# Optimization experiments

Hardware: AMD Instinct MI355X
Metric: run time of the kernel (lower is better)

Reference implementation:

```python
import jax, jax.numpy as jnp
import numpy as np

DIM = 256
HEADS = 8
WH, WW = 8, 8
N = WH * WW
B_ = 2048
NW = 64  # num windows per image; B_ // NW = batch of 32
CPB_HIDDEN = 256


def _log_rel_index(wh, ww):
    ch = np.arange(wh)
    cw = np.arange(ww)
    coords = np.stack(np.meshgrid(ch, cw, indexing='ij'))      # (2, wh, ww)
    cf = coords.reshape(2, -1)                                  # (2, N)
    rel = cf[:, :, None] - cf[:, None, :]                       # (2, N, N)
    rel = rel.transpose(1, 2, 0).astype(np.float32)             # (N, N, 2)
    return np.sign(rel) * np.log1p(np.abs(rel))


def setup_inputs() -> dict:
    key = jax.random.key(0)
    ks = jax.random.split(key, 16)
    s = 0.02
    inp = {
        'x': jax.random.normal(ks[0], (B_, N, DIM), jnp.float32),
        'KV': jax.random.normal(ks[1], (B_, N, DIM), jnp.float32),
        'mask': jnp.zeros((NW, N, N), jnp.float32),
        # linear weights stored (in, out): y = x @ W + b
        'Wq': jax.random.normal(ks[2], (DIM, DIM), jnp.float32) * s,
        'bq': jnp.zeros((DIM,), jnp.float32),
        'Wkv': jax.random.normal(ks[3], (DIM, 2 * DIM), jnp.float32) * s,
        'bkv': jnp.zeros((2 * DIM,), jnp.float32),
        'Wp': jax.random.normal(ks[4], (DIM, DIM), jnp.float32) * s,
        'bp': jnp.zeros((DIM,), jnp.float32),
        'cpb_w1': jax.random.normal(ks[5], (2, CPB_HIDDEN), jnp.float32) * s,
        'cpb_b1': jnp.zeros((CPB_HIDDEN,), jnp.float32),
        'cpb_w2': jax.random.normal(ks[6], (CPB_HIDDEN, HEADS), jnp.float32) * s,
        'cpb_b2': jnp.zeros((HEADS,), jnp.float32),
        'tau': jnp.ones((HEADS, N, N), jnp.float32),
        'log_rel_idx': jnp.asarray(_log_rel_index(WH, WW)),  # (N, N, 2)
    }
    return inp


def reference(x, KV, mask, Wq, bq, Wkv, bkv, Wp, bp,
              cpb_w1, cpb_b1, cpb_w2, cpb_b2, tau, log_rel_idx):
    Bw, n, C = x.shape
    H = tau.shape[0]
    hd = C // H
    scale = hd ** -0.5

    q = (x @ Wq + bq).reshape(Bw, n, H, hd).transpose(0, 2, 1, 3) * scale   # (B_,H,N,hd)
    kv = (KV @ Wkv + bkv).reshape(Bw, n, 2, H, hd).transpose(2, 0, 3, 1, 4)  # (2,B_,H,N,hd)
    k, v = kv[0], kv[1]

    num = jnp.einsum('bhqd,bhkd->bhqk', q, k)
    qn = jnp.sqrt(jnp.sum(q * q, axis=-1, keepdims=True))                    # (B_,H,N,1)
    kn = jnp.sqrt(jnp.sum(k * k, axis=-1, keepdims=True))                    # (B_,H,N,1)
    denom = jnp.maximum(qn * kn.transpose(0, 1, 3, 2), 1e-6)
    attn = num / denom
    attn = attn / jnp.clip(tau[:, :n, :n], 0.01)[None]

    # continuous relative position bias MLP: (N,N,2) -> (N,N,H)
    h = jax.nn.relu(log_rel_idx[:n, :n] @ cpb_w1 + cpb_b1)
    bias = (h @ cpb_w2 + cpb_b2).transpose(2, 0, 1)                          # (H,N,N)
    attn = attn + bias[None]

    nW = mask.shape[0]
    attn = attn.reshape(Bw // nW, nW, H, n, n) + mask[None, :, None]
    attn = attn.reshape(Bw, H, n, n)
    attn = jax.nn.softmax(attn, axis=-1)

    out = jnp.einsum('bhqk,bhkd->bhqd', attn, v)
    out = out.transpose(0, 2, 1, 3).reshape(Bw, n, C)
    out = out @ Wp + bp
    return out
```

## Files before the change

kernel.cpp:

```cpp
#include <hip/hip_runtime.h>
#include <hip/hip_bf16.h>

#define NWIN 64

typedef __attribute__((ext_vector_type(8))) short v8s;
typedef __attribute__((ext_vector_type(4))) float v4f;

#define WQT_OFF   0u
#define WKVT_OFF  131072u
#define WPT_OFF   393216u
#define ITB_OFF   524288u

static __device__ __forceinline__ short f2bf(float f) {
  union { float f; unsigned int u; } v; v.f = f;
  unsigned int u = v.u;
  return (short)((u + 0x7fffu + ((u >> 16) & 1u)) >> 16);
}

static __device__ __forceinline__ int packbf(float lo, float hi) {
  __hip_bfloat162 h = __float22bfloat162_rn(float2{lo, hi});
  union { __hip_bfloat162 h; int i; } u; u.h = h; return u.i;
}

__global__ void prep_kernel(const float* __restrict__ Wq, const float* __restrict__ Wkv,
                            const float* __restrict__ Wp,
                            short* __restrict__ WqT, short* __restrict__ WkvT,
                            short* __restrict__ WpT) {
  int id = blockIdx.x * 256 + threadIdx.x;
  if (id < 65536) {
    int o = id >> 8, i = id & 255;
    WqT[id] = f2bf(Wq[i * 256 + o]);
  } else if (id < 196608) {
    int t = id - 65536; int o = t >> 8, i = t & 255;
    WkvT[t] = f2bf(Wkv[i * 512 + o]);
  } else if (id < 262144) {
    int t = id - 196608; int o = t >> 8, i = t & 255;
    WpT[t] = f2bf(Wp[i * 256 + o]);
  }
}

__global__ void cpb_kernel(const float* __restrict__ w1, const float* __restrict__ b1,
                           const float* __restrict__ w2, const float* __restrict__ b2,
                           const float* __restrict__ lri, const float* __restrict__ tau,
                           unsigned int* __restrict__ itbh) {
  int ij = blockIdx.x * 256 + threadIdx.x;
  float l0 = lri[ij * 2], l1 = lri[ij * 2 + 1];
  float acc[8];
#pragma unroll
  for (int h = 0; h < 8; ++h) acc[h] = b2[h];
  for (int c = 0; c < 256; ++c) {
    float hv = fmaxf(l0 * w1[c] + l1 * w1[256 + c] + b1[c], 0.0f);
#pragma unroll
    for (int h = 0; h < 8; ++h) acc[h] += hv * w2[c * 8 + h];
  }
#pragma unroll
  for (int h = 0; h < 8; ++h) {
    float it = 1.0f / fmaxf(tau[h * 4096 + ij], 0.01f);
    itbh[h * 4096 + ij] = (unsigned int)packbf(it, acc[h]);
  }
}

static __device__ __forceinline__ v8s xform_tile(int p0a, int p0b, int p1a, int p1b,
                                                 int base, int mdsel) {
  int a0 = __shfl(p0a, base, 64),      b0 = __shfl(p1a, base, 64);
  int a1 = __shfl(p0b, base, 64),      b1 = __shfl(p1b, base, 64);
  int a2 = __shfl(p0a, base + 16, 64), b2 = __shfl(p1a, base + 16, 64);
  int a3 = __shfl(p0b, base + 16, 64), b3 = __shfl(p1b, base + 16, 64);
  union { v8s v; int i[4]; } r;
  r.i[0] = mdsel ? b0 : a0;
  r.i[1] = mdsel ? b1 : a1;
  r.i[2] = mdsel ? b2 : a2;
  r.i[3] = mdsel ? b3 : a3;
  return r.v;
}

__global__ __launch_bounds__(512, 4) void wattn_kernel(
    const float* __restrict__ x, const float* __restrict__ KV,
    const float* __restrict__ mask,
    const float* __restrict__ bq, const float* __restrict__ bkv,
    const float* __restrict__ bp,
    const short* __restrict__ WqT, const short* __restrict__ WkvT,
    const short* __restrict__ WpT, const unsigned int* __restrict__ itbh,
    float* __restrict__ out) {
  __shared__ short sm[37888];

  const int b = blockIdx.x;
  const int tid = threadIdx.x;
  const int w = tid >> 6;
  const int lane = tid & 63;
  const int cc = lane & 15;
  const int qd = lane >> 4;
  const int base = cc + 32 * (qd & 1);
  const int mdsel = qd >> 1;
  const v4f vzero = {0.f, 0.f, 0.f, 0.f};
  short* xs = sm;
  short* kvs = sm + 16896;
  short* ms = sm + 33792;

  {
    const float4* xb = (const float4*)(x + (size_t)b * 16384);
    const float4* kb = (const float4*)(KV + (size_t)b * 16384);
    const float4* mb = (const float4*)(mask + (size_t)(b & (NWIN - 1)) * 4096);
    float4 m0 = mb[tid * 2], m1 = mb[tid * 2 + 1];
#pragma unroll
    for (int half = 0; half < 2; ++half) {
      float4 vx[4], vk[4];
#pragma unroll
      for (int ii = 0; ii < 4; ++ii) {
        int i = tid + (half * 4 + ii) * 512;
        vx[ii] = xb[i];
        vk[ii] = kb[i];
      }
#pragma unroll
      for (int ii = 0; ii < 4; ++ii) {
        int i = tid + (half * 4 + ii) * 512;
        int r = i >> 6, col = (i & 63) << 2;
        int2 px = { packbf(vx[ii].x, vx[ii].y), packbf(vx[ii].z, vx[ii].w) };
        int2 pk = { packbf(vk[ii].x, vk[ii].y), packbf(vk[ii].z, vk[ii].w) };
        *(int2*)&xs[r * 264 + col] = px;
        *(int2*)&kvs[r * 264 + col] = pk;
      }
    }
    int byte = (tid * 16) ^ (((tid >> 3) & 7) << 3);
    int2 p0 = { packbf(m0.x, m0.y), packbf(m0.z, m0.w) };
    int2 p1 = { packbf(m1.x, m1.y), packbf(m1.z, m1.w) };
    *(int2*)((char*)ms + byte) = p0;
    *(int2*)((char*)ms + (byte ^ 8)) = p1;
  }
  const short* wqb = WqT + (32 * w + cc) * 256 + qd * 8;
  v8s wq0[4], wq1[4];
#pragma unroll
  for (int it = 0; it < 4; ++it) {
    wq0[it] = *(const v8s*)(wqb + it * 32);
    wq1[it] = *(const v8s*)(wqb + 16 * 256 + it * 32);
  }
  __syncthreads();

  v4f Dq[2][4];
#pragma unroll
  for (int md = 0; md < 2; ++md)
#pragma unroll
    for (int nt = 0; nt < 4; ++nt) Dq[md][nt] = vzero;
  {
#pragma unroll
    for (int it = 0; it < 4; ++it) {
#pragma unroll
      for (int nt = 0; nt < 4; ++nt) {
        v8s bx = *(const v8s*)(xs + (nt * 16 + cc) * 264 + it * 32 + qd * 8);
        Dq[0][nt] = __builtin_amdgcn_mfma_f32_16x16x32_bf16(wq0[it], bx, Dq[0][nt], 0, 0, 0);
        Dq[1][nt] = __builtin_amdgcn_mfma_f32_16x16x32_bf16(wq1[it], bx, Dq[1][nt], 0, 0, 0);
      }
    }
#pragma unroll
    for (int it = 4; it < 8; ++it) {
      v8s a0 = *(const v8s*)(wqb + it * 32);
      v8s a1 = *(const v8s*)(wqb + 16 * 256 + it * 32);
#pragma unroll
      for (int nt = 0; nt < 4; ++nt) {
        v8s bx = *(const v8s*)(xs + (nt * 16 + cc) * 264 + it * 32 + qd * 8);
        Dq[0][nt] = __builtin_amdgcn_mfma_f32_16x16x32_bf16(a0, bx, Dq[0][nt], 0, 0, 0);
        Dq[1][nt] = __builtin_amdgcn_mfma_f32_16x16x32_bf16(a1, bx, Dq[1][nt], 0, 0, 0);
      }
    }
  }
  v8s qB[4];
  {
    v4f b0 = *(const v4f*)(bq + 32 * w + qd * 4);
    v4f b1 = *(const v4f*)(bq + 32 * w + 16 + qd * 4);
#pragma unroll
    for (int nt = 0; nt < 4; ++nt) {
      float s = 0.f;
#pragma unroll
      for (int rg = 0; rg < 4; ++rg) {
        float v0 = Dq[0][nt][rg] + b0[rg];
        float v1 = Dq[1][nt][rg] + b1[rg];
        Dq[0][nt][rg] = v0; Dq[1][nt][rg] = v1;
        s += v0 * v0 + v1 * v1;
      }
      s += __shfl_xor(s, 16); s += __shfl_xor(s, 32);
      float inv = rsqrtf(s + 1e-24f);
      int p00 = packbf(Dq[0][nt][0] * inv, Dq[0][nt][1] * inv);
      int p01 = packbf(Dq[0][nt][2] * inv, Dq[0][nt][3] * inv);
      int p10 = packbf(Dq[1][nt][0] * inv, Dq[1][nt][1] * inv);
      int p11 = packbf(Dq[1][nt][2] * inv, Dq[1][nt][3] * inv);
      qB[nt] = xform_tile(p00, p01, p10, p11, base, mdsel);
    }
  }

  v4f Dk[2][4], Dv[4][2];
#pragma unroll
  for (int nt = 0; nt < 4; ++nt) {
    Dk[0][nt] = vzero; Dk[1][nt] = vzero;
    Dv[nt][0] = vzero; Dv[nt][1] = vzero;
  }
  {
    const short* wkb = WkvT + (32 * w + cc) * 256 + qd * 8;
    const short* wvb = WkvT + (256 + 32 * w + cc) * 256 + qd * 8;
#pragma unroll
    for (int it = 0; it < 8; ++it) {
      v8s ak0 = *(const v8s*)(wkb + it * 32);
      v8s ak1 = *(const v8s*)(wkb + 16 * 256 + it * 32);
      v8s bv0 = *(const v8s*)(wvb + it * 32);
      v8s bv1 = *(const v8s*)(wvb + 16 * 256 + it * 32);
#pragma unroll
      for (int nt = 0; nt < 4; ++nt) {
        v8s kf = *(const v8s*)(kvs + (nt * 16 + cc) * 264 + it * 32 + qd * 8);
        Dk[0][nt] = __builtin_amdgcn_mfma_f32_16x16x32_bf16(ak0, kf, Dk[0][nt], 0, 0, 0);
        Dk[1][nt] = __builtin_amdgcn_mfma_f32_16x16x32_bf16(ak1, kf, Dk[1][nt], 0, 0, 0);
        Dv[nt][0] = __builtin_amdgcn_mfma_f32_16x16x32_bf16(kf, bv0, Dv[nt][0], 0, 0, 0);
        Dv[nt][1] = __builtin_amdgcn_mfma_f32_16x16x32_bf16(kf, bv1, Dv[nt][1], 0, 0, 0);
      }
    }
  }
  v8s kA[4];
  {
    v4f b0 = *(const v4f*)(bkv + 32 * w + qd * 4);
    v4f b1 = *(const v4f*)(bkv + 32 * w + 16 + qd * 4);
#pragma unroll
    for (int nt = 0; nt < 4; ++nt) {
      float s = 0.f;
#pragma unroll
      for (int rg = 0; rg < 4; ++rg) {
        float v0 = Dk[0][nt][rg] + b0[rg];
        float v1 = Dk[1][nt][rg] + b1[rg];
        Dk[0][nt][rg] = v0; Dk[1][nt][rg] = v1;
        s += v0 * v0 + v1 * v1;
      }
      s += __shfl_xor(s, 16); s += __shfl_xor(s, 32);
      float inv = rsqrtf(s + 1e-24f);
      int p00 = packbf(Dk[0][nt][0] * inv, Dk[0][nt][1] * inv);
      int p01 = packbf(Dk[0][nt][2] * inv, Dk[0][nt][3] * inv);
      int p10 = packbf(Dk[1][nt][0] * inv, Dk[1][nt][1] * inv);
      int p11 = packbf(Dk[1][nt][2] * inv, Dk[1][nt][3] * inv);
      kA[nt] = xform_tile(p00, p01, p10, p11, base, mdsel);
    }
  }
  v8s av[2][2];
  {
    float bv0 = bkv[256 + 32 * w + cc];
    float bv1 = bkv[256 + 32 * w + 16 + cc];
    int Pv[4][2][2];
#pragma unroll
    for (int vt = 0; vt < 4; ++vt) {
      Pv[vt][0][0] = packbf(Dv[vt][0][0] + bv0, Dv[vt][0][1] + bv0);
      Pv[vt][0][1] = packbf(Dv[vt][0][2] + bv0, Dv[vt][0][3] + bv0);
      Pv[vt][1][0] = packbf(Dv[vt][1][0] + bv1, Dv[vt][1][1] + bv1);
      Pv[vt][1][1] = packbf(Dv[vt][1][2] + bv1, Dv[vt][1][3] + bv1);
    }
#pragma unroll
    for (int md = 0; md < 2; ++md)
#pragma unroll
      for (int kc = 0; kc < 2; ++kc)
        av[md][kc] = xform_tile(Pv[2 * kc][md][0], Pv[2 * kc][md][1],
                                Pv[2 * kc + 1][md][0], Pv[2 * kc + 1][md][1], base, mdsel);
  }

  v4f Sv[4][4];
  __builtin_amdgcn_s_setprio(1);
#pragma unroll
  for (int jt = 0; jt < 4; ++jt)
#pragma unroll
    for (int it = 0; it < 4; ++it)
      Sv[jt][it] = __builtin_amdgcn_mfma_f32_16x16x32_bf16(kA[jt], qB[it], vzero, 0, 0, 0);
  __builtin_amdgcn_s_setprio(0);

  {
    const uint4* th4 = (const uint4*)(itbh + (size_t)w * 4096);
#pragma unroll
    for (int it = 0; it < 4; ++it) {
      int i = it * 16 + cc;
      uint4 T[4]; int2 M[4];
#pragma unroll
      for (int jt = 0; jt < 4; ++jt) {
        T[jt] = th4[(i * 64 + jt * 16 + qd * 4) >> 2];
        int byte = (i * 128 + jt * 32 + qd * 8) ^ ((i & 7) << 3);
        M[jt] = *(const int2*)((const char*)ms + byte);
      }
#pragma unroll
      for (int jt = 0; jt < 4; ++jt) {
        unsigned mxw = (unsigned)M[jt].x, myw = (unsigned)M[jt].y;
        float m0 = __uint_as_float(mxw << 16);
        float m1 = __uint_as_float(mxw & 0xffff0000u);
        float m2 = __uint_as_float(myw << 16);
        float m3 = __uint_as_float(myw & 0xffff0000u);
        unsigned u0 = T[jt].x, u1 = T[jt].y, u2 = T[jt].z, u3 = T[jt].w;
        Sv[jt][it][0] = Sv[jt][it][0] * __uint_as_float(u0 << 16) + (__uint_as_float(u0 & 0xffff0000u) + m0);
        Sv[jt][it][1] = Sv[jt][it][1] * __uint_as_float(u1 << 16) + (__uint_as_float(u1 & 0xffff0000u) + m1);
        Sv[jt][it][2] = Sv[jt][it][2] * __uint_as_float(u2 << 16) + (__uint_as_float(u2 & 0xffff0000u) + m2);
        Sv[jt][it][3] = Sv[jt][it][3] * __uint_as_float(u3 << 16) + (__uint_as_float(u3 & 0xffff0000u) + m3);
      }
      float mA = fmaxf(fmaxf(Sv[0][it][0], Sv[0][it][1]), fmaxf(Sv[0][it][2], Sv[0][it][3]));
      float mB = fmaxf(fmaxf(Sv[1][it][0], Sv[1][it][1]), fmaxf(Sv[1][it][2], Sv[1][it][3]));
      float mC = fmaxf(fmaxf(Sv[2][it][0], Sv[2][it][1]), fmaxf(Sv[2][it][2], Sv[2][it][3]));
      float mD = fmaxf(fmaxf(Sv[3][it][0], Sv[3][it][1]), fmaxf(Sv[3][it][2], Sv[3][it][3]));
      float mx = fmaxf(fmaxf(mA, mB), fmaxf(mC, mD));
      mx = fmaxf(mx, __shfl_xor(mx, 16)); mx = fmaxf(mx, __shfl_xor(mx, 32));
      float sj[4];
#pragma unroll
      for (int jt = 0; jt < 4; ++jt) {
        float e0 = __expf(Sv[jt][it][0] - mx);
        float e1 = __expf(Sv[jt][it][1] - mx);
        float e2 = __expf(Sv[jt][it][2] - mx);
        float e3 = __expf(Sv[jt][it][3] - mx);
        Sv[jt][it][0] = e0; Sv[jt][it][1] = e1;
        Sv[jt][it][2] = e2; Sv[jt][it][3] = e3;
        sj[jt] = (e0 + e1) + (e2 + e3);
      }
      float sum = (sj[0] + sj[1]) + (sj[2] + sj[3]);
      sum += __shfl_xor(sum, 16); sum += __shfl_xor(sum, 32);
      float rs = 1.0f / sum;
#pragma unroll
      for (int jt = 0; jt < 4; ++jt)
#pragma unroll
        for (int rg = 0; rg < 4; ++rg) Sv[jt][it][rg] *= rs;
    }
  }

  __syncthreads();
  v4f Do[2][4];
  {
    char* psw = (char*)kvs + w * 4096;
#pragma unroll
    for (int it = 0; it < 4; ++it) {
      char* ps = psw + (it & 1) * 2048;
#pragma unroll
      for (int jt = 0; jt < 4; ++jt) {
        int2 pr;
        pr.x = packbf(Sv[jt][it][0], Sv[jt][it][1]);
        pr.y = packbf(Sv[jt][it][2], Sv[jt][it][3]);
        int byte = (cc * 128 + jt * 32 + qd * 8) ^ ((cc & 7) << 4);
        *(int2*)(ps + byte) = pr;
      }
      int rb0 = (cc * 128 + qd * 16) ^ ((cc & 7) << 4);
      int rb1 = (cc * 128 + 64 + qd * 16) ^ ((cc & 7) << 4);
      v8s pB0 = *(const v8s*)(ps + rb0);
      v8s pB1 = *(const v8s*)(ps + rb1);
      __builtin_amdgcn_s_setprio(1);
#pragma unroll
      for (int md = 0; md < 2; ++md) {
        v4f t = __builtin_amdgcn_mfma_f32_16x16x32_bf16(av[md][0], pB0, vzero, 0, 0, 0);
        Do[md][it] = __builtin_amdgcn_mfma_f32_16x16x32_bf16(av[md][1], pB1, t, 0, 0, 0);
      }
      __builtin_amdgcn_s_setprio(0);
    }
  }

  const short* wpb = WpT + (32 * w + cc) * 256 + qd * 8;
  v8s wp0[2], wp1[2];
#pragma unroll
  for (int it = 0; it < 2; ++it) {
    wp0[it] = *(const v8s*)(wpb + it * 32);
    wp1[it] = *(const v8s*)(wpb + 16 * 256 + it * 32);
  }

#pragma unroll
  for (int md = 0; md < 2; ++md)
#pragma unroll
    for (int it = 0; it < 4; ++it) {
      int addr = (it * 16 + cc) * 264 + 32 * w + md * 16 + qd * 4;
      *(int*)&sm[addr] = packbf(Do[md][it][0], Do[md][it][1]);
      *(int*)&sm[addr + 2] = packbf(Do[md][it][2], Do[md][it][3]);
    }
  __syncthreads();

  v4f pa[4][2];
#pragma unroll
  for (int mt = 0; mt < 4; ++mt) { pa[mt][0] = vzero; pa[mt][1] = vzero; }
  {
#pragma unroll
    for (int it = 0; it < 2; ++it) {
#pragma unroll
      for (int mt = 0; mt < 4; ++mt) {
        v8s a = *(const v8s*)(sm + (mt * 16 + cc) * 264 + it * 32 + qd * 8);
        pa[mt][0] = __builtin_amdgcn_mfma_f32_16x16x32_bf16(a, wp0[it], pa[mt][0], 0, 0, 0);
        pa[mt][1] = __builtin_amdgcn_mfma_f32_16x16x32_bf16(a, wp1[it], pa[mt][1], 0, 0, 0);
      }
    }
#pragma unroll
    for (int it = 2; it < 8; ++it) {
      v8s b0 = *(const v8s*)(wpb + it * 32);
      v8s b1 = *(const v8s*)(wpb + 16 * 256 + it * 32);
#pragma unroll
      for (int mt = 0; mt < 4; ++mt) {
        v8s a = *(const v8s*)(sm + (mt * 16 + cc) * 264 + it * 32 + qd * 8);
        pa[mt][0] = __builtin_amdgcn_mfma_f32_16x16x32_bf16(a, b0, pa[mt][0], 0, 0, 0);
        pa[mt][1] = __builtin_amdgcn_mfma_f32_16x16x32_bf16(a, b1, pa[mt][1], 0, 0, 0);
      }
    }
  }
  {
    float b0 = bp[32 * w + cc], b1 = bp[32 * w + 16 + cc];
    float* ob = out + (size_t)b * 16384;
#pragma unroll
    for (int mt = 0; mt < 4; ++mt)
#pragma unroll
      for (int rg = 0; rg < 4; ++rg) {
        int row = mt * 16 + qd * 4 + rg;
        ob[row * 256 + 32 * w + cc] = pa[mt][0][rg] + b0;
        ob[row * 256 + 32 * w + 16 + cc] = pa[mt][1][rg] + b1;
      }
  }
}

extern "C" void kernel_launch(void* const* d_in, const int* in_sizes, int n_in,
                              void* d_out, int out_size, void* d_ws, size_t ws_size,
                              hipStream_t stream) {
  const float* x    = (const float*)d_in[0];
  const float* KV   = (const float*)d_in[1];
  const float* mask = (const float*)d_in[2];
  const float* Wq   = (const float*)d_in[3];
  const float* bq   = (const float*)d_in[4];
  const float* Wkv  = (const float*)d_in[5];
  const float* bkv  = (const float*)d_in[6];
  const float* Wp   = (const float*)d_in[7];
  const float* bp   = (const float*)d_in[8];
  const float* cw1  = (const float*)d_in[9];
  const float* cb1  = (const float*)d_in[10];
  const float* cw2  = (const float*)d_in[11];
  const float* cb2  = (const float*)d_in[12];
  const float* tau  = (const float*)d_in[13];
  const float* lri  = (const float*)d_in[14];

  unsigned char* ws = (unsigned char*)d_ws;
  short* WqT   = (short*)(ws + WQT_OFF);
  short* WkvT  = (short*)(ws + WKVT_OFF);
  short* WpT   = (short*)(ws + WPT_OFF);
  unsigned int* itbh = (unsigned int*)(ws + ITB_OFF);

  prep_kernel<<<1024, 256, 0, stream>>>(Wq, Wkv, Wp, WqT, WkvT, WpT);
  cpb_kernel<<<16, 256, 0, stream>>>(cw1, cb1, cw2, cb2, lri, tau, itbh);
  wattn_kernel<<<2048, 512, 0, stream>>>(x, KV, mask, bq, bkv, bp,
                                         WqT, WkvT, WpT, itbh, (float*)d_out);
}
```

Before: 507.7 us.

## Make attention kernel persistent over four windows with x prefetch double-buffering

Launches 512 blocks that each process four windows in a loop, swapping two shared-memory buffers. The next window's x tile is loaded from global memory and written to the spare buffer while the output projection runs. The aim is to cut block launch overhead and hide x load latency. The cost is fewer resident blocks per CU, and the KV load for later windows is not overlapped with compute.

```diff
diff --git a/kernel.cpp b/kernel.cpp
--- a/kernel.cpp
+++ b/kernel.cpp
@@ -84,7 +84,7 @@
     float* __restrict__ out) {
   __shared__ short sm[37888];
 
-  const int b = blockIdx.x;
+  const int b0 = blockIdx.x;
   const int tid = threadIdx.x;
   const int w = tid >> 6;
   const int lane = tid & 63;
@@ -93,14 +93,19 @@
   const int base = cc + 32 * (qd & 1);
   const int mdsel = qd >> 1;
   const v4f vzero = {0.f, 0.f, 0.f, 0.f};
-  short* xs = sm;
-  short* kvs = sm + 16896;
   short* ms = sm + 33792;
+  short* pX = sm;
+  short* pK = sm + 16896;
+
+  const short* wqb = WqT + (32 * w + cc) * 256 + qd * 8;
+  const short* wkb = WkvT + (32 * w + cc) * 256 + qd * 8;
+  const short* wvb = WkvT + (256 + 32 * w + cc) * 256 + qd * 8;
+  const short* wpb = WpT + (32 * w + cc) * 256 + qd * 8;
 
   {
-    const float4* xb = (const float4*)(x + (size_t)b * 16384);
-    const float4* kb = (const float4*)(KV + (size_t)b * 16384);
-    const float4* mb = (const float4*)(mask + (size_t)(b & (NWIN - 1)) * 4096);
+    const float4* xb = (const float4*)(x + (size_t)b0 * 16384);
+    const float4* kb = (const float4*)(KV + (size_t)b0 * 16384);
+    const float4* mb = (const float4*)(mask + (size_t)(b0 & (NWIN - 1)) * 4096);
     float4 m0 = mb[tid * 2], m1 = mb[tid * 2 + 1];
 #pragma unroll
     for (int half = 0; half < 2; ++half) {
@@ -117,8 +122,8 @@
         int r = i >> 6, col = (i & 63) << 2;
         int2 px = { packbf(vx[ii].x, vx[ii].y), packbf(vx[ii].z, vx[ii].w) };
         int2 pk = { packbf(vk[ii].x, vk[ii].y), packbf(vk[ii].z, vk[ii].w) };
-        *(int2*)&xs[r * 264 + col] = px;
-        *(int2*)&kvs[r * 264 + col] = pk;
+        *(int2*)&pX[r * 264 + col] = px;
+        *(int2*)&pK[r * 264 + col] = pk;
       }
     }
     int byte = (tid * 16) ^ (((tid >> 3) & 7) << 3);
@@ -127,278 +132,340 @@
     *(int2*)((char*)ms + byte) = p0;
     *(int2*)((char*)ms + (byte ^ 8)) = p1;
   }
-  const short* wqb = WqT + (32 * w + cc) * 256 + qd * 8;
-  v8s wq0[4], wq1[4];
-#pragma unroll
-  for (int it = 0; it < 4; ++it) {
-    wq0[it] = *(const v8s*)(wqb + it * 32);
-    wq1[it] = *(const v8s*)(wqb + 16 * 256 + it * 32);
-  }
-  __syncthreads();
-
-  v4f Dq[2][4];
-#pragma unroll
-  for (int md = 0; md < 2; ++md)
-#pragma unroll
-    for (int nt = 0; nt < 4; ++nt) Dq[md][nt] = vzero;
-  {
+
+#pragma unroll 1
+  for (int wi = 0; wi < 4; ++wi) {
+    const int b = b0 + wi * 512;
+
+    if (wi > 0) {
+      const float4* kb = (const float4*)(KV + (size_t)b * 16384);
+      float4 kf[8];
+#pragma unroll
+      for (int c = 0; c < 8; ++c) kf[c] = kb[tid + c * 512];
+#pragma unroll
+      for (int c = 0; c < 8; ++c) {
+        int i = tid + c * 512;
+        int r = i >> 6, col = (i & 63) << 2;
+        int2 pk = { packbf(kf[c].x, kf[c].y), packbf(kf[c].z, kf[c].w) };
+        *(int2*)&pK[r * 264 + col] = pk;
+      }
+    }
+    v8s wq0[4], wq1[4];
 #pragma unroll
     for (int it = 0; it < 4; ++it) {
+      wq0[it] = *(const v8s*)(wqb + it * 32);
+      wq1[it] = *(const v8s*)(wqb + 16 * 256 + it * 32);
+    }
+    __syncthreads();
+
+    v4f Dq[2][4];
+#pragma unroll
+    for (int md = 0; md < 2; ++md)
+#pragma unroll
+      for (int nt = 0; nt < 4; ++nt) Dq[md][nt] = vzero;
+    {
+#pragma unroll
+      for (int it = 0; it < 4; ++it) {
+#pragma unroll
+        for (int nt = 0; nt < 4; ++nt) {
+          v8s bx = *(const v8s*)(pX + (nt * 16 + cc) * 264 + it * 32 + qd * 8);
+          Dq[0][nt] = __builtin_amdgcn_mfma_f32_16x16x32_bf16(wq0[it], bx, Dq[0][nt], 0, 0, 0);
+          Dq[1][nt] = __builtin_amdgcn_mfma_f32_16x16x32_bf16(wq1[it], bx, Dq[1][nt], 0, 0, 0);
+        }
+      }
+#pragma unroll
+      for (int it = 4; it < 8; ++it) {
+        v8s a0 = *(const v8s*)(wqb + it * 32);
+        v8s a1 = *(const v8s*)(wqb + 16 * 256 + it * 32);
+#pragma unroll
+        for (int nt = 0; nt < 4; ++nt) {
+          v8s bx = *(const v8s*)(pX + (nt * 16 + cc) * 264 + it * 32 + qd * 8);
+          Dq[0][nt] = __builtin_amdgcn_mfma_f32_16x16x32_bf16(a0, bx, Dq[0][nt], 0, 0, 0);
+          Dq[1][nt] = __builtin_amdgcn_mfma_f32_16x16x32_bf16(a1, bx, Dq[1][nt], 0, 0, 0);
+        }
+      }
+    }
+    v8s qB[4];
+    {
+      v4f bb0 = *(const v4f*)(bq + 32 * w + qd * 4);
+      v4f bb1 = *(const v4f*)(bq + 32 * w + 16 + qd * 4);
 #pragma unroll
       for (int nt = 0; nt < 4; ++nt) {
-        v8s bx = *(const v8s*)(xs + (nt * 16 + cc) * 264 + it * 32 + qd * 8);
-        Dq[0][nt] = __builtin_amdgcn_mfma_f32_16x16x32_bf16(wq0[it], bx, Dq[0][nt], 0, 0, 0);
-        Dq[1][nt] = __builtin_amdgcn_mfma_f32_16x16x32_bf16(wq1[it], bx, Dq[1][nt], 0, 0, 0);
-      }
-    }
-#pragma unroll
-    for (int it = 4; it < 8; ++it) {
-      v8s a0 = *(const v8s*)(wqb + it * 32);
-      v8s a1 = *(const v8s*)(wqb + 16 * 256 + it * 32);
+        float s = 0.f;
+#pragma unroll
+        for (int rg = 0; rg < 4; ++rg) {
+          float v0 = Dq[0][nt][rg] + bb0[rg];
+          float v1 = Dq[1][nt][rg] + bb1[rg];
+          Dq[0][nt][rg] = v0; Dq[1][nt][rg] = v1;
+          s += v0 * v0 + v1 * v1;
+        }
+        s += __shfl_xor(s, 16); s += __shfl_xor(s, 32);
+        float inv = rsqrtf(s + 1e-24f);
+        int p00 = packbf(Dq[0][nt][0] * inv, Dq[0][nt][1] * inv);
+        int p01 = packbf(Dq[0][nt][2] * inv, Dq[0][nt][3] * inv);
+        int p10 = packbf(Dq[1][nt][0] * inv, Dq[1][nt][1] * inv);
+        int p11 = packbf(Dq[1][nt][2] * inv, Dq[1][nt][3] * inv);
+        qB[nt] = xform_tile(p00, p01, p10, p11, base, mdsel);
+      }
+    }
+
+    v4f Dk[2][4], Dv[4][2];
+#pragma unroll
+    for (int nt = 0; nt < 4; ++nt) {
+      Dk[0][nt] = vzero; Dk[1][nt] = vzero;
+      Dv[nt][0] = vzero; Dv[nt][1] = vzero;
+    }
+    {
+#pragma unroll
+      for (int it = 0; it < 8; ++it) {
+        v8s ak0 = *(const v8s*)(wkb + it * 32);
+        v8s ak1 = *(const v8s*)(wkb + 16 * 256 + it * 32);
+        v8s bv0 = *(const v8s*)(wvb + it * 32);
+        v8s bv1 = *(const v8s*)(wvb + 16 * 256 + it * 32);
+#pragma unroll
+        for (int nt = 0; nt < 4; ++nt) {
+          v8s kf = *(const v8s*)(pK + (nt * 16 + cc) * 264 + it * 32 + qd * 8);
+          Dk[0][nt] = __builtin_amdgcn_mfma_f32_16x16x32_bf16(ak0, kf, Dk[0][nt], 0, 0, 0);
+          Dk[1][nt] = __builtin_amdgcn_mfma_f32_16x16x32_bf16(ak1, kf, Dk[1][nt], 0, 0, 0);
+          Dv[nt][0] = __builtin_amdgcn_mfma_f32_16x16x32_bf16(kf, bv0, Dv[nt][0], 0, 0, 0);
+          Dv[nt][1] = __builtin_amdgcn_mfma_f32_16x16x32_bf16(kf, bv1, Dv[nt][1], 0, 0, 0);
+        }
+      }
+    }
+    v8s kA[4];
+    {
+      v4f bb0 = *(const v4f*)(bkv + 32 * w + qd * 4);
+      v4f bb1 = *(const v4f*)(bkv + 32 * w + 16 + qd * 4);
 #pragma unroll
       for (int nt = 0; nt < 4; ++nt) {
-        v8s bx = *(const v8s*)(xs + (nt * 16 + cc) * 264 + it * 32 + qd * 8);
-        Dq[0][nt] = __builtin_amdgcn_mfma_f32_16x16x32_bf16(a0, bx, Dq[0][nt], 0, 0, 0);
-        Dq[1][nt] = __builtin_amdgcn_mfma_f32_16x16x32_bf16(a1, bx, Dq[1][nt], 0, 0, 0);
-      }
-    }
-  }
-  v8s qB[4];
-  {
-    v4f b0 = *(const v4f*)(bq + 32 * w + qd * 4);
-    v4f b1 = *(const v4f*)(bq + 32 * w + 16 + qd * 4);
-#pragma unroll
-    for (int nt = 0; nt < 4; ++nt) {
-      float s = 0.f;
-#pragma unroll
-      for (int rg = 0; rg < 4; ++rg) {
-        float v0 = Dq[0][nt][rg] + b0[rg];
-        float v1 = Dq[1][nt][rg] + b1[rg];
-        Dq[0][nt][rg] = v0; Dq[1][nt][rg] = v1;
-        s += v0 * v0 + v1 * v1;
-      }
-      s += __shfl_xor(s, 16); s += __shfl_xor(s, 32);
-      float inv = rsqrtf(s + 1e-24f);
-      int p00 = packbf(Dq[0][nt][0] * inv, Dq[0][nt][1] * inv);
-      int p01 = packbf(Dq[0][nt][2] * inv, Dq[0][nt][3] * inv);
-      int p10 = packbf(Dq[1][nt][0] * inv, Dq[1][nt][1] * inv);
-      int p11 = packbf(Dq[1][nt][2] * inv, Dq[1][nt][3] * inv);
-      qB[nt] = xform_tile(p00, p01, p10, p11, base, mdsel);
-    }
-  }
-
-  v4f Dk[2][4], Dv[4][2];
-#pragma unroll
-  for (int nt = 0; nt < 4; ++nt) {
-    Dk[0][nt] = vzero; Dk[1][nt] = vzero;
-    Dv[nt][0] = vzero; Dv[nt][1] = vzero;
-  }
-  {
-    const short* wkb = WkvT + (32 * w + cc) * 256 + qd * 8;
-    const short* wvb = WkvT + (256 + 32 * w + cc) * 256 + qd * 8;
-#pragma unroll
-    for (int it = 0; it < 8; ++it) {
-      v8s ak0 = *(const v8s*)(wkb + it * 32);
-      v8s ak1 = *(const v8s*)(wkb + 16 * 256 + it * 32);
-      v8s bv0 = *(const v8s*)(wvb + it * 32);
-      v8s bv1 = *(const v8s*)(wvb + 16 * 256 + it * 32);
-#pragma unroll
-      for (int nt = 0; nt < 4; ++nt) {
-        v8s kf = *(const v8s*)(kvs + (nt * 16 + cc) * 264 + it * 32 + qd * 8);
-        Dk[0][nt] = __builtin_amdgcn_mfma_f32_16x16x32_bf16(ak0, kf, Dk[0][nt], 0, 0, 0);
-        Dk[1][nt] = __builtin_amdgcn_mfma_f32_16x16x32_bf16(ak1, kf, Dk[1][nt], 0, 0, 0);
-        Dv[nt][0] = __builtin_amdgcn_mfma_f32_16x16x32_bf16(kf, bv0, Dv[nt][0], 0, 0, 0);
-        Dv[nt][1] = __builtin_amdgcn_mfma_f32_16x16x32_bf16(kf, bv1, Dv[nt][1], 0, 0, 0);
-      }
-    }
-  }
-  v8s kA[4];
-  {
-    v4f b0 = *(const v4f*)(bkv + 32 * w + qd * 4);
-    v4f b1 = *(const v4f*)(bkv + 32 * w + 16 + qd * 4);
-#pragma unroll
-    for (int nt = 0; nt < 4; ++nt) {
-      float s = 0.f;
-#pragma unroll
-      for (int rg = 0; rg < 4; ++rg) {
-        float v0 = Dk[0][nt][rg] + b0[rg];
-        float v1 = Dk[1][nt][rg] + b1[rg];
-        Dk[0][nt][rg] = v0; Dk[1][nt][rg] = v1;
-        s += v0 * v0 + v1 * v1;
-      }
-      s += __shfl_xor(s, 16); s += __shfl_xor(s, 32);
-      float inv = rsqrtf(s + 1e-24f);
-      int p00 = packbf(Dk[0][nt][0] * inv, Dk[0][nt][1] * inv);
-      int p01 = packbf(Dk[0][nt][2] * inv, Dk[0][nt][3] * inv);
-      int p10 = packbf(Dk[1][nt][0] * inv, Dk[1][nt][1] * inv);
-      int p11 = packbf(Dk[1][nt][2] * inv, Dk[1][nt][3] * inv);
-      kA[nt] = xform_tile(p00, p01, p10, p11, base, mdsel);
-    }
-  }
-  v8s av[2][2];
-  {
-    float bv0 = bkv[256 + 32 * w + cc];
-    float bv1 = bkv[256 + 32 * w + 16 + cc];
-    int Pv[4][2][2];
-#pragma unroll
-    for (int vt = 0; vt < 4; ++vt) {
-      Pv[vt][0][0] = packbf(Dv[vt][0][0] + bv0, Dv[vt][0][1] + bv0);
-      Pv[vt][0][1] = packbf(Dv[vt][0][2] + bv0, Dv[vt][0][3] + bv0);
-      Pv[vt][1][0] = packbf(Dv[vt][1][0] + bv1, Dv[vt][1][1] + bv1);
-      Pv[vt][1][1] = packbf(Dv[vt][1][2] + bv1, Dv[vt][1][3] + bv1);
-    }
+        float s = 0.f;
+#pragma unroll
+        for (int rg = 0; rg < 4; ++rg) {
+          float v0 = Dk[0][nt][rg] + bb0[rg];
+          float v1 = Dk[1][nt][rg] + bb1[rg];
+          Dk[0][nt][rg] = v0; Dk[1][nt][rg] = v1;
+          s += v0 * v0 + v1 * v1;
+        }
+        s += __shfl_xor(s, 16); s += __shfl_xor(s, 32);
+        float inv = rsqrtf(s + 1e-24f);
+        int p00 = packbf(Dk[0][nt][0] * inv, Dk[0][nt][1] * inv);
+        int p01 = packbf(Dk[0][nt][2] * inv, Dk[0][nt][3] * inv);
+        int p10 = packbf(Dk[1][nt][0] * inv, Dk[1][nt][1] * inv);
+        int p11 = packbf(Dk[1][nt][2] * inv, Dk[1][nt][3] * inv);
+        kA[nt] = xform_tile(p00, p01, p10, p11, base, mdsel);
+      }
+    }
+    v8s av[2][2];
+    {
+      float bv0 = bkv[256 + 32 * w + cc];
+      float bv1 = bkv[256 + 32 * w + 16 + cc];
+      int Pv[4][2][2];
+#pragma unroll
+      for (int vt = 0; vt < 4; ++vt) {
+        Pv[vt][0][0] = packbf(Dv[vt][0][0] + bv0, Dv[vt][0][1] + bv0);
+        Pv[vt][0][1] = packbf(Dv[vt][0][2] + bv0, Dv[vt][0][3] + bv0);
+        Pv[vt][1][0] = packbf(Dv[vt][1][0] + bv1, Dv[vt][1][1] + bv1);
+        Pv[vt][1][1] = packbf(Dv[vt][1][2] + bv1, Dv[vt][1][3] + bv1);
+      }
+#pragma unroll
+      for (int md = 0; md < 2; ++md)
+#pragma unroll
+        for (int kc = 0; kc < 2; ++kc)
+          av[md][kc] = xform_tile(Pv[2 * kc][md][0], Pv[2 * kc][md][1],
+                                  Pv[2 * kc + 1][md][0], Pv[2 * kc + 1][md][1], base, mdsel);
+    }
+
+    v4f Sv[4][4];
+    __builtin_amdgcn_s_setprio(1);
+#pragma unroll
+    for (int jt = 0; jt < 4; ++jt)
+#pragma unroll
+      for (int it = 0; it < 4; ++it)
+        Sv[jt][it] = __builtin_amdgcn_mfma_f32_16x16x32_bf16(kA[jt], qB[it], vzero, 0, 0, 0);
+    __builtin_amdgcn_s_setprio(0);
+
+    {
+      const uint4* th4 = (const uint4*)(itbh + (size_t)w * 4096);
+#pragma unroll
+      for (int it = 0; it < 4; ++it) {
+        int i = it * 16 + cc;
+        uint4 T[4]; int2 M[4];
+#pragma unroll
+        for (int jt = 0; jt < 4; ++jt) {
+          T[jt] = th4[(i * 64 + jt * 16 + qd * 4) >> 2];
+          int byte = (i * 128 + jt * 32 + qd * 8) ^ ((i & 7) << 3);
+          M[jt] = *(const int2*)((const char*)ms + byte);
+        }
+#pragma unroll
+        for (int jt = 0; jt < 4; ++jt) {
+          unsigned mxw = (unsigned)M[jt].x, myw = (unsigned)M[jt].y;
+          float m0 = __uint_as_float(mxw << 16);
+          float m1 = __uint_as_float(mxw & 0xffff0000u);
+          float m2 = __uint_as_float(myw << 16);
+          float m3 = __uint_as_float(myw & 0xffff0000u);
+          unsigned u0 = T[jt].x, u1 = T[jt].y, u2 = T[jt].z, u3 = T[jt].w;
+          Sv[jt][it][0] = Sv[jt][it][0] * __uint_as_float(u0 << 16) + (__uint_as_float(u0 & 0xffff0000u) + m0);
+          Sv[jt][it][1] = Sv[jt][it][1] * __uint_as_float(u1 << 16) + (__uint_as_float(u1 & 0xffff0000u) + m1);
+          Sv[jt][it][2] = Sv[jt][it][2] * __uint_as_float(u2 << 16) + (__uint_as_float(u2 & 0xffff0000u) + m2);
+          Sv[jt][it][3] = Sv[jt][it][3] * __uint_as_float(u3 << 16) + (__uint_as_float(u3 & 0xffff0000u) + m3);
+        }
+        float mA = fmaxf(fmaxf(Sv[0][it][0], Sv[0][it][1]), fmaxf(Sv[0][it][2], Sv[0][it][3]));
+        float mB = fmaxf(fmaxf(Sv[1][it][0], Sv[1][it][1]), fmaxf(Sv[1][it][2], Sv[1][it][3]));
+        float mC = fmaxf(fmaxf(Sv[2][it][0], Sv[2][it][1]), fmaxf(Sv[2][it][2], Sv[2][it][3]));
+        float mD = fmaxf(fmaxf(Sv[3][it][0], Sv[3][it][1]), fmaxf(Sv[3][it][2], Sv[3][it][3]));
+        float mx = fmaxf(fmaxf(mA, mB), fmaxf(mC, mD));
+        mx = fmaxf(mx, __shfl_xor(mx, 16)); mx = fmaxf(mx, __shfl_xor(mx, 32));
+        float sj[4];
+#pragma unroll
+        for (int jt = 0; jt < 4; ++jt) {
+          float e0 = __expf(Sv[jt][it][0] - mx);
+          float e1 = __expf(Sv[jt][it][1] - mx);
+          float e2 = __expf(Sv[jt][it][2] - mx);
+          float e3 = __expf(Sv[jt][it][3] - mx);
+          Sv[jt][it][0] = e0; Sv[jt][it][1] = e1;
+          Sv[jt][it][2] = e2; Sv[jt][it][3] = e3;
+          sj[jt] = (e0 + e1) + (e2 + e3);
+        }
+        float sum = (sj[0] + sj[1]) + (sj[2] + sj[3]);
+        sum += __shfl_xor(sum, 16); sum += __shfl_xor(sum, 32);
+        float rs = 1.0f / sum;
+#pragma unroll
+        for (int jt = 0; jt < 4; ++jt)
+#pragma unroll
+          for (int rg = 0; rg < 4; ++rg) Sv[jt][it][rg] *= rs;
+      }
+    }
+
+    __syncthreads();
+    v4f Do[2][4];
+    {
+      char* psw = (char*)pK + w * 4096;
+#pragma unroll
+      for (int it = 0; it < 4; ++it) {
+        char* ps = psw + (it & 1) * 2048;
+#pragma unroll
+        for (int jt = 0; jt < 4; ++jt) {
+          int2 pr;
+          pr.x = packbf(Sv[jt][it][0], Sv[jt][it][1]);
+          pr.y = packbf(Sv[jt][it][2], Sv[jt][it][3]);
+          int byte = (cc * 128 + jt * 32 + qd * 8) ^ ((cc & 7) << 4);
+          *(int2*)(ps + byte) = pr;
+        }
+        int rb0 = (cc * 128 + qd * 16) ^ ((cc & 7) << 4);
+        int rb1 = (cc * 128 + 64 + qd * 16) ^ ((cc & 7) << 4);
+        v8s pB0 = *(const v8s*)(ps + rb0);
+        v8s pB1 = *(const v8s*)(ps + rb1);
+        __builtin_amdgcn_s_setprio(1);
+#pragma unroll
+        for (int md = 0; md < 2; ++md) {
+          v4f t = __builtin_amdgcn_mfma_f32_16x16x32_bf16(av[md][0], pB0, vzero, 0, 0, 0);
+          Do[md][it] = __builtin_amdgcn_mfma_f32_16x16x32_bf16(av[md][1], pB1, t, 0, 0, 0);
+        }
+        __builtin_amdgcn_s_setprio(0);
+      }
+    }
+
+    v8s wp0[2], wp1[2];
+#pragma unroll
+    for (int it = 0; it < 2; ++it) {
+      wp0[it] = *(const v8s*)(wpb + it * 32);
+      wp1[it] = *(const v8s*)(wpb + 16 * 256 + it * 32);
+    }
+
 #pragma unroll
     for (int md = 0; md < 2; ++md)
 #pragma unroll
-      for (int kc = 0; kc < 2; ++kc)
-        av[md][kc] = xform_tile(Pv[2 * kc][md][0], Pv[2 * kc][md][1],
-                                Pv[2 * kc + 1][md][0], Pv[2 * kc + 1][md][1], base, mdsel);
-  }
-
-  v4f Sv[4][4];
-  __builtin_amdgcn_s_setprio(1);
-#pragma unroll
-  for (int jt = 0; jt < 4; ++jt)
-#pragma unroll
-    for (int it = 0; it < 4; ++it)
-      Sv[jt][it] = __builtin_amdgcn_mfma_f32_16x16x32_bf16(kA[jt], qB[it], vzero, 0, 0, 0);
-  __builtin_amdgcn_s_setprio(0);
-
-  {
-    const uint4* th4 = (const uint4*)(itbh + (size_t)w * 4096);
-#pragma unroll
-    for (int it = 0; it < 4; ++it) {
-      int i = it * 16 + cc;
-      uint4 T[4]; int2 M[4];
-#pragma unroll
-      for (int jt = 0; jt < 4; ++jt) {
-        T[jt] = th4[(i * 64 + jt * 16 + qd * 4) >> 2];
-        int byte = (i * 128 + jt * 32 + qd * 8) ^ ((i & 7) << 3);
-        M[jt] = *(const int2*)((const char*)ms + byte);
-      }
-#pragma unroll
-      for (int jt = 0; jt < 4; ++jt) {
-        unsigned mxw = (unsigned)M[jt].x, myw = (unsigned)M[jt].y;
-        float m0 = __uint_as_float(mxw << 16);
-        float m1 = __uint_as_float(mxw & 0xffff0000u);
-        float m2 = __uint_as_float(myw << 16);
-        float m3 = __uint_as_float(myw & 0xffff0000u);
-        unsigned u0 = T[jt].x, u1 = T[jt].y, u2 = T[jt].z, u3 = T[jt].w;
-        Sv[jt][it][0] = Sv[jt][it][0] * __uint_as_float(u0 << 16) + (__uint_as_float(u0 & 0xffff0000u) + m0);
-        Sv[jt][it][1] = Sv[jt][it][1] * __uint_as_float(u1 << 16) + (__uint_as_float(u1 & 0xffff0000u) + m1);
-        Sv[jt][it][2] = Sv[jt][it][2] * __uint_as_float(u2 << 16) + (__uint_as_float(u2 & 0xffff0000u) + m2);
-        Sv[jt][it][3] = Sv[jt][it][3] * __uint_as_float(u3 << 16) + (__uint_as_float(u3 & 0xffff0000u) + m3);
-      }
-      float mA = fmaxf(fmaxf(Sv[0][it][0], Sv[0][it][1]), fmaxf(Sv[0][it][2], Sv[0][it][3]));
-      float mB = fmaxf(fmaxf(Sv[1][it][0], Sv[1][it][1]), fmaxf(Sv[1][it][2], Sv[1][it][3]));
-      float mC = fmaxf(fmaxf(Sv[2][it][0], Sv[2][it][1]), fmaxf(Sv[2][it][2], Sv[2][it][3]));
-      float mD = fmaxf(fmaxf(Sv[3][it][0], Sv[3][it][1]), fmaxf(Sv[3][it][2], Sv[3][it][3]));
-      float mx = fmaxf(fmaxf(mA, mB), fmaxf(mC, mD));
-      mx = fmaxf(mx, __shfl_xor(mx, 16)); mx = fmaxf(mx, __shfl_xor(mx, 32));
-      float sj[4];
-#pragma unroll
-      for (int jt = 0; jt < 4; ++jt) {
-        float e0 = __expf(Sv[jt][it][0] - mx);
-        float e1 = __expf(Sv[jt][it][1] - mx);
-        float e2 = __expf(Sv[jt][it][2] - mx);
-        float e3 = __expf(Sv[jt][it][3] - mx);
-        Sv[jt][it][0] = e0; Sv[jt][it][1] = e1;
-        Sv[jt][it][2] = e2; Sv[jt][it][3] = e3;
-        sj[jt] = (e0 + e1) + (e2 + e3);
-      }
-      float sum = (sj[0] + sj[1]) + (sj[2] + sj[3]);
-      sum += __shfl_xor(sum, 16); sum += __shfl_xor(sum, 32);
-      float rs = 1.0f / sum;
-#pragma unroll
-      for (int jt = 0; jt < 4; ++jt)
-#pragma unroll
-        for (int rg = 0; rg < 4; ++rg) Sv[jt][it][rg] *= rs;
-    }
-  }
-
-  __syncthreads();
-  v4f Do[2][4];
-  {
-    char* psw = (char*)kvs + w * 4096;
-#pragma unroll
-    for (int it = 0; it < 4; ++it) {
-      char* ps = psw + (it & 1) * 2048;
-#pragma unroll
-      for (int jt = 0; jt < 4; ++jt) {
-        int2 pr;
-        pr.x = packbf(Sv[jt][it][0], Sv[jt][it][1]);
-        pr.y = packbf(Sv[jt][it][2], Sv[jt][it][3]);
-        int byte = (cc * 128 + jt * 32 + qd * 8) ^ ((cc & 7) << 4);
-        *(int2*)(ps + byte) = pr;
-      }
-      int rb0 = (cc * 128 + qd * 16) ^ ((cc & 7) << 4);
-      int rb1 = (cc * 128 + 64 + qd * 16) ^ ((cc & 7) << 4);
-      v8s pB0 = *(const v8s*)(ps + rb0);
-      v8s pB1 = *(const v8s*)(ps + rb1);
-      __builtin_amdgcn_s_setprio(1);
-#pragma unroll
-      for (int md = 0; md < 2; ++md) {
-        v4f t = __builtin_amdgcn_mfma_f32_16x16x32_bf16(av[md][0], pB0, vzero, 0, 0, 0);
-        Do[md][it] = __builtin_amdgcn_mfma_f32_16x16x32_bf16(av[md][1], pB1, t, 0, 0, 0);
-      }
-      __builtin_amdgcn_s_setprio(0);
-    }
-  }
-
-  const short* wpb = WpT + (32 * w + cc) * 256 + qd * 8;
-  v8s wp0[2], wp1[2];
-#pragma unroll
-  for (int it = 0; it < 2; ++it) {
-    wp0[it] = *(const v8s*)(wpb + it * 32);
-    wp1[it] = *(const v8s*)(wpb + 16 * 256 + it * 32);
-  }
-
-#pragma unroll
-  for (int md = 0; md < 2; ++md)
-#pragma unroll
-    for (int it = 0; it < 4; ++it) {
-      int addr = (it * 16 + cc) * 264 + 32 * w + md * 16 + qd * 4;
-      *(int*)&sm[addr] = packbf(Do[md][it][0], Do[md][it][1]);
-      *(int*)&sm[addr + 2] = packbf(Do[md][it][2], Do[md][it][3]);
-    }
-  __syncthreads();
-
-  v4f pa[4][2];
-#pragma unroll
-  for (int mt = 0; mt < 4; ++mt) { pa[mt][0] = vzero; pa[mt][1] = vzero; }
-  {
-#pragma unroll
-    for (int it = 0; it < 2; ++it) {
-#pragma unroll
-      for (int mt = 0; mt < 4; ++mt) {
-        v8s a = *(const v8s*)(sm + (mt * 16 + cc) * 264 + it * 32 + qd * 8);
-        pa[mt][0] = __builtin_amdgcn_mfma_f32_16x16x32_bf16(a, wp0[it], pa[mt][0], 0, 0, 0);
-        pa[mt][1] = __builtin_amdgcn_mfma_f32_16x16x32_bf16(a, wp1[it], pa[mt][1], 0, 0, 0);
-      }
-    }
-#pragma unroll
-    for (int it = 2; it < 8; ++it) {
-      v8s b0 = *(const v8s*)(wpb + it * 32);
-      v8s b1 = *(const v8s*)(wpb + 16 * 256 + it * 32);
-#pragma unroll
-      for (int mt = 0; mt < 4; ++mt) {
-        v8s a = *(const v8s*)(sm + (mt * 16 + cc) * 264 + it * 32 + qd * 8);
-        pa[mt][0] = __builtin_amdgcn_mfma_f32_16x16x32_bf16(a, b0, pa[mt][0], 0, 0, 0);
-        pa[mt][1] = __builtin_amdgcn_mfma_f32_16x16x32_bf16(a, b1, pa[mt][1], 0, 0, 0);
-      }
-    }
-  }
-  {
-    float b0 = bp[32 * w + cc], b1 = bp[32 * w + 16 + cc];
-    float* ob = out + (size_t)b * 16384;
-#pragma unroll
-    for (int mt = 0; mt < 4; ++mt)
-#pragma unroll
-      for (int rg = 0; rg < 4; ++rg) {
-        int row = mt * 16 + qd * 4 + rg;
-        ob[row * 256 + 32 * w + cc] = pa[mt][0][rg] + b0;
-        ob[row * 256 + 32 * w + 16 + cc] = pa[mt][1][rg] + b1;
-      }
+      for (int it = 0; it < 4; ++it) {
+        int addr = (it * 16 + cc) * 264 + 32 * w + md * 16 + qd * 4;
+        *(int*)&pX[addr] = packbf(Do[md][it][0], Do[md][it][1]);
+        *(int*)&pX[addr + 2] = packbf(Do[md][it][2], Do[md][it][3]);
+      }
+    __syncthreads();
+
+    const float4* xbn = (const float4*)(x + (size_t)(b + 512) * 16384);
+    float4 xf0, xf1, xf2, xf3;
+    if (wi < 3) {
+      xf0 = xbn[tid];       xf1 = xbn[tid + 512];
+      xf2 = xbn[tid + 1024]; xf3 = xbn[tid + 1536];
+    }
+
+    v4f pa[4][2];
+#pragma unroll
+    for (int mt = 0; mt < 4; ++mt) { pa[mt][0] = vzero; pa[mt][1] = vzero; }
+    {
+#pragma unroll
+      for (int it = 0; it < 2; ++it) {
+#pragma unroll
+        for (int mt = 0; mt < 4; ++mt) {
+          v8s a = *(const v8s*)(pX + (mt * 16 + cc) * 264 + it * 32 + qd * 8);
+          pa[mt][0] = __builtin_amdgcn_mfma_f32_16x16x32_bf16(a, wp0[it], pa[mt][0], 0, 0, 0);
+          pa[mt][1] = __builtin_amdgcn_mfma_f32_16x16x32_bf16(a, wp1[it], pa[mt][1], 0, 0, 0);
+        }
+      }
+#pragma unroll
+      for (int it = 2; it < 4; ++it) {
+        v8s bw0 = *(const v8s*)(wpb + it * 32);
+        v8s bw1 = *(const v8s*)(wpb + 16 * 256 + it * 32);
+#pragma unroll
+        for (int mt = 0; mt < 4; ++mt) {
+          v8s a = *(const v8s*)(pX + (mt * 16 + cc) * 264 + it * 32 + qd * 8);
+          pa[mt][0] = __builtin_amdgcn_mfma_f32_16x16x32_bf16(a, bw0, pa[mt][0], 0, 0, 0);
+          pa[mt][1] = __builtin_amdgcn_mfma_f32_16x16x32_bf16(a, bw1, pa[mt][1], 0, 0, 0);
+        }
+      }
+    }
+    float4 xf4, xf5, xf6, xf7;
+    if (wi < 3) {
+      xf4 = xbn[tid + 2048]; xf5 = xbn[tid + 2560];
+      xf6 = xbn[tid + 3072]; xf7 = xbn[tid + 3584];
+#pragma unroll
+      for (int c = 0; c < 4; ++c) {
+        float4 v = (c == 0) ? xf0 : (c == 1) ? xf1 : (c == 2) ? xf2 : xf3;
+        int i = tid + c * 512;
+        int r = i >> 6, col = (i & 63) << 2;
+        int2 px = { packbf(v.x, v.y), packbf(v.z, v.w) };
+        *(int2*)&pK[r * 264 + col] = px;
+      }
+    }
+    {
+#pragma unroll
+      for (int it = 4; it < 8; ++it) {
+        v8s bw0 = *(const v8s*)(wpb + it * 32);
+        v8s bw1 = *(const v8s*)(wpb + 16 * 256 + it * 32);
+#pragma unroll
+        for (int mt = 0; mt < 4; ++mt) {
+          v8s a = *(const v8s*)(pX + (mt * 16 + cc) * 264 + it * 32 + qd * 8);
+          pa[mt][0] = __builtin_amdgcn_mfma_f32_16x16x32_bf16(a, bw0, pa[mt][0], 0, 0, 0);
+          pa[mt][1] = __builtin_amdgcn_mfma_f32_16x16x32_bf16(a, bw1, pa[mt][1], 0, 0, 0);
+        }
+      }
+    }
+    if (wi < 3) {
+#pragma unroll
+      for (int c = 4; c < 8; ++c) {
+        float4 v = (c == 4) ? xf4 : (c == 5) ? xf5 : (c == 6) ? xf6 : xf7;
+        int i = tid + c * 512;
+        int r = i >> 6, col = (i & 63) << 2;
+        int2 px = { packbf(v.x, v.y), packbf(v.z, v.w) };
+        *(int2*)&pK[r * 264 + col] = px;
+      }
+    }
+
+    {
+      float bb0 = bp[32 * w + cc], bb1 = bp[32 * w + 16 + cc];
+      float* ob = out + (size_t)b * 16384;
+#pragma unroll
+      for (int mt = 0; mt < 4; ++mt)
+#pragma unroll
+        for (int rg = 0; rg < 4; ++rg) {
+          int row = mt * 16 + qd * 4 + rg;
+          ob[row * 256 + 32 * w + cc] = pa[mt][0][rg] + bb0;
+          ob[row * 256 + 32 * w + 16 + cc] = pa[mt][1][rg] + bb1;
+        }
+    }
+
+    __syncthreads();
+    { short* t = pX; pX = pK; pK = t; }
   }
 }
 
@@ -429,6 +496,6 @@
 
   prep_kernel<<<1024, 256, 0, stream>>>(Wq, Wkv, Wp, WqT, WkvT, WpT);
   cpb_kernel<<<16, 256, 0, stream>>>(cw1, cb1, cw2, cb2, lri, tau, itbh);
-  wattn_kernel<<<2048, 512, 0, stream>>>(x, KV, mask, bq, bkv, bp,
-                                         WqT, WkvT, WpT, itbh, (float*)d_out);
-}
+  wattn_kernel<<<512, 512, 0, stream>>>(x, KV, mask, bq, bkv, bp,
+                                        WqT, WkvT, WpT, itbh, (float*)d_out);
+}
```

After: 1.058 ms. 2.08x slower.
